# Kernel optimization log

Measured on AMD Instinct MI355X. Metric: run time of the kernel, lower is better.

The kernel has to match this reference:

```python
import jax, jax.numpy as jnp
import numpy as np

B, N, D, H = 8, 1024, 768, 12
HD = D // H


def setup_inputs() -> dict:
    key = jax.random.key(0)
    ks = jax.random.split(key, 13)
    s = 0.02
    return {
        "q": jax.random.normal(ks[0], (B, N, D), jnp.float32),
        "k": jax.random.normal(ks[1], (B, N, D), jnp.float32),
        "v": jax.random.normal(ks[2], (B, N, D), jnp.float32),
        "attn_bias": jax.random.normal(ks[3], (B, H, N, N), jnp.float32),
        "attn_mask": jnp.ones((B, N, N), jnp.int32),
        "Wq": jax.random.normal(ks[4], (D, D), jnp.float32) * s,
        "bq": jnp.zeros((D,), jnp.float32),
        "Wk": jax.random.normal(ks[5], (D, D), jnp.float32) * s,
        "bk": jnp.zeros((D,), jnp.float32),
        "Wv": jax.random.normal(ks[6], (D, D), jnp.float32) * s,
        "bv": jnp.zeros((D,), jnp.float32),
        "Wo": jax.random.normal(ks[7], (D, D), jnp.float32) * s,
        "bo": jnp.zeros((D,), jnp.float32),
    }


def reference(q, k, v, attn_bias, attn_mask, Wq, bq, Wk, bk, Wv, bv, Wo, bo):
    scale = jnp.sqrt(jnp.float32(HD))
    # projections; nn.Linear computes x @ W.T + b
    qh = (q @ Wq.T + bq).reshape(B, N, H, HD).transpose(0, 2, 1, 3)  # [B,H,N,hd]
    kh = (k @ Wk.T + bk).reshape(B, N, H, HD).transpose(0, 2, 1, 3)
    vh = (v @ Wv.T + bv).reshape(B, N, H, HD).transpose(0, 2, 1, 3)
    attn = jnp.einsum("bhqd,bhkd->bhqk", qh, kh) / scale
    attn = attn + attn_bias  # Graphormer edge/spatial bias
    attn = jnp.where(attn_mask[:, None, :, :] == 0, -jnp.inf, attn)
    attn = jax.nn.softmax(attn, axis=-1)
    out = jnp.einsum("bhqk,bhkd->bhqd", attn, vh)  # [B,H,N,hd]
    out = out.transpose(0, 2, 1, 3).reshape(B, N, D)
    return out @ Wo.T + bo
```

## Files before the change

### kernel.cpp

```cpp
#include <hip/hip_runtime.h>
#include <hip/hip_bf16.h>

using f32x4  = __attribute__((ext_vector_type(4))) float;
using i32x4  = __attribute__((ext_vector_type(4))) int;
using bf16x8 = __attribute__((ext_vector_type(8))) short;
using bf16x4 = __attribute__((ext_vector_type(4))) short;

constexpr int BATCH = 8, SEQ = 1024, DIM = 768, NHEAD = 12, HDIM = 64;
constexpr int MROWS = BATCH * SEQ;

__device__ __forceinline__ short f2bf(float f) {
    union { float f; unsigned u; } x; x.f = f;
    unsigned r = (x.u + 0x7fffu + ((x.u >> 16) & 1u)) >> 16;
    return (short)r;
}
__device__ __forceinline__ float fexp2(float x) { return __builtin_amdgcn_exp2f(x); }

template <typename AT, int OMODE>
__global__ __launch_bounds__(256)
void gemm_bt(const AT* __restrict__ A, const float* __restrict__ W,
             const float* __restrict__ bias, void* __restrict__ Cout, float oscale) {
    constexpr int K  = DIM;
    constexpr int NT = DIM / 128;
    __shared__ short As[128][72];
    __shared__ short Bs[128][72];

    const int bm = blockIdx.x / NT, bn = blockIdx.x % NT;
    const int m0 = bm * 128, n0 = bn * 128;
    const int t = threadIdx.x;
    const int lane = t & 63, w = t >> 6;
    const int wm = (w >> 1) * 64, wn = (w & 1) * 64;
    const int l16 = lane & 15, lg = lane >> 4;

    const int sr = t >> 1, sc = (t & 1) * 16;

    f32x4 acc[4][4] = {};

    for (int k0 = 0; k0 < K; k0 += 32) {
        __syncthreads();
        if constexpr (sizeof(AT) == 4) {
            const float* ap = (const float*)A + (long)(m0 + sr) * K + k0 + sc;
            float tmp[16];
            *(f32x4*)&tmp[0]  = *(const f32x4*)(ap + 0);
            *(f32x4*)&tmp[4]  = *(const f32x4*)(ap + 4);
            *(f32x4*)&tmp[8]  = *(const f32x4*)(ap + 8);
            *(f32x4*)&tmp[12] = *(const f32x4*)(ap + 12);
            short tb[16];
            #pragma unroll
            for (int j = 0; j < 16; ++j) tb[j] = f2bf(tmp[j]);
            *(bf16x8*)&As[sr][sc]     = *(bf16x8*)&tb[0];
            *(bf16x8*)&As[sr][sc + 8] = *(bf16x8*)&tb[8];
        } else {
            const short* ap = (const short*)A + (long)(m0 + sr) * K + k0 + sc;
            *(bf16x8*)&As[sr][sc]     = *(const bf16x8*)(ap);
            *(bf16x8*)&As[sr][sc + 8] = *(const bf16x8*)(ap + 8);
        }
        {
            const float* wp = W + (long)(n0 + sr) * K + k0 + sc;
            float tmp[16];
            *(f32x4*)&tmp[0]  = *(const f32x4*)(wp + 0);
            *(f32x4*)&tmp[4]  = *(const f32x4*)(wp + 4);
            *(f32x4*)&tmp[8]  = *(const f32x4*)(wp + 8);
            *(f32x4*)&tmp[12] = *(const f32x4*)(wp + 12);
            short tb[16];
            #pragma unroll
            for (int j = 0; j < 16; ++j) tb[j] = f2bf(tmp[j]);
            *(bf16x8*)&Bs[sr][sc]     = *(bf16x8*)&tb[0];
            *(bf16x8*)&Bs[sr][sc + 8] = *(bf16x8*)&tb[8];
        }
        __syncthreads();

        bf16x8 af[4], bfg[4];
        const int kc = lg * 8;
        #pragma unroll
        for (int mi = 0; mi < 4; ++mi)
            af[mi] = *(const bf16x8*)&As[wm + mi * 16 + l16][kc];
        #pragma unroll
        for (int ni = 0; ni < 4; ++ni)
            bfg[ni] = *(const bf16x8*)&Bs[wn + ni * 16 + l16][kc];
        #pragma unroll
        for (int mi = 0; mi < 4; ++mi)
            #pragma unroll
            for (int ni = 0; ni < 4; ++ni)
                acc[mi][ni] = __builtin_amdgcn_mfma_f32_16x16x32_bf16(
                    af[mi], bfg[ni], acc[mi][ni], 0, 0, 0);
    }

    #pragma unroll
    for (int mi = 0; mi < 4; ++mi) {
        const int row = m0 + wm + mi * 16 + lg * 4;
        #pragma unroll
        for (int ni = 0; ni < 4; ++ni) {
            const int col = n0 + wn + ni * 16 + l16;
            const float bv = bias[col];
            #pragma unroll
            for (int j = 0; j < 4; ++j) {
                float val = (acc[mi][ni][j] + bv) * oscale;
                if constexpr (OMODE == 0) {
                    ((short*)Cout)[(long)(row + j) * DIM + col] = f2bf(val);
                } else if constexpr (OMODE == 1) {
                    ((float*)Cout)[(long)(row + j) * DIM + col] = val;
                } else {
                    const int bb = row / SEQ;
                    const int tok = (row % SEQ) + j;
                    const int hh = col >> 6, dd = col & 63;
                    const long base = ((long)(bb * NHEAD + hh) * 16 + (tok >> 6)) * 4096;
                    if constexpr (OMODE == 2)
                        ((short*)Cout)[base + dd * 64 + (tok & 63)] = f2bf(val);
                    else
                        ((short*)Cout)[base + (tok & 63) * 64 + dd] = f2bf(val);
                }
            }
        }
    }
}

__global__ __launch_bounds__(256)
void attn_kernel(const short* __restrict__ Qp, const short* __restrict__ Kt,
                 const short* __restrict__ Vt, const float* __restrict__ bias,
                 const int* __restrict__ mask, short* __restrict__ Op) {
    __shared__ float Bsm[64][68];
    __shared__ short Ks[64][72];
    __shared__ short Vs[64][72];
    __shared__ short Ps[4][16][72];

    const int d = blockIdx.x;
    const int lgc = (d & 7) * 192 + (d >> 3);
    const int qt = lgc & 15, pair = lgc >> 4;
    const int h = pair % NHEAD, b = pair / NHEAD;

    const int t = threadIdx.x, lane = t & 63, w = t >> 6;
    const int l16 = lane & 15, lg = lane >> 4;
    const int ql = w * 16 + l16;

    const int qrow = qt * 64 + ql;
    const short* qptr = Qp + (long)(b * SEQ + qrow) * DIM + h * HDIM + lg * 8;
    const bf16x8 qf0 = *(const bf16x8*)qptr;
    const bf16x8 qf1 = *(const bf16x8*)(qptr + 32);

    const short* ktile = Kt + (long)pair * 16 * 4096;
    const short* vtile = Vt + (long)pair * 16 * 4096;

    const int srow = t >> 4, scol = (t & 15) * 4;
    const float* bst = bias + ((long)pair * SEQ + qt * 64 + srow) * SEQ + scol;
    const int*   mst = mask + ((long)b * SEQ + qt * 64 + srow) * SEQ + scol;

    const int kr = t >> 3, kc = (t & 7) * 8;

    f32x4 acc_o[4] = {};
    float m_run = -1e30f, l_run = 0.f;
    constexpr float L2E = 1.4426950408889634f;

    f32x4 br[4]; i32x4 mr[4]; bf16x8 kst0, kst1, vst0, vst1;

    {
        #pragma unroll
        for (int i = 0; i < 4; ++i) {
            br[i] = *(const f32x4*)(bst + (long)i * 16 * SEQ);
            mr[i] = *(const i32x4*)(mst + (long)i * 16 * SEQ);
        }
        kst0 = *(const bf16x8*)(ktile + t * 8);
        kst1 = *(const bf16x8*)(ktile + t * 8 + 2048);
        vst0 = *(const bf16x8*)(vtile + t * 8);
        vst1 = *(const bf16x8*)(vtile + t * 8 + 2048);
        #pragma unroll
        for (int i = 0; i < 4; ++i) {
            f32x4 o;
            #pragma unroll
            for (int j = 0; j < 4; ++j) o[j] = mr[i][j] ? br[i][j] : -1e30f;
            *(f32x4*)&Bsm[i * 16 + srow][scol] = o;
        }
        *(bf16x8*)&Ks[kr][kc]      = kst0;
        *(bf16x8*)&Ks[kr + 32][kc] = kst1;
        *(bf16x8*)&Vs[kr][kc]      = vst0;
        *(bf16x8*)&Vs[kr + 32][kc] = vst1;
    }
    __syncthreads();

    for (int kt = 0; kt < 16; ++kt) {
        if (kt < 15) {
            #pragma unroll
            for (int i = 0; i < 4; ++i) {
                br[i] = *(const f32x4*)(bst + (long)i * 16 * SEQ + (kt + 1) * 64);
                mr[i] = *(const i32x4*)(mst + (long)i * 16 * SEQ + (kt + 1) * 64);
            }
            const short* kp = ktile + (kt + 1) * 4096 + t * 8;
            const short* vp = vtile + (kt + 1) * 4096 + t * 8;
            kst0 = *(const bf16x8*)kp;
            kst1 = *(const bf16x8*)(kp + 2048);
            vst0 = *(const bf16x8*)vp;
            vst1 = *(const bf16x8*)(vp + 2048);
        }

        f32x4 s[4];
        #pragma unroll
        for (int c = 0; c < 4; ++c) {
            const bf16x8 kb0 = *(const bf16x8*)&Ks[c * 16 + l16][lg * 8];
            const bf16x8 kb1 = *(const bf16x8*)&Ks[c * 16 + l16][32 + lg * 8];
            f32x4 ci = *(const f32x4*)&Bsm[ql][c * 16 + lg * 4];
            ci   = __builtin_amdgcn_mfma_f32_16x16x32_bf16(kb0, qf0, ci, 0, 0, 0);
            s[c] = __builtin_amdgcn_mfma_f32_16x16x32_bf16(kb1, qf1, ci, 0, 0, 0);
        }

        bf16x8 vb0[4], vb1[4];
        #pragma unroll
        for (int df = 0; df < 4; ++df) {
            vb0[df] = *(const bf16x8*)&Vs[df * 16 + l16][lg * 8];
            vb1[df] = *(const bf16x8*)&Vs[df * 16 + l16][32 + lg * 8];
        }

        float mt = -1e30f;
        #pragma unroll
        for (int c = 0; c < 4; ++c)
            #pragma unroll
            for (int j = 0; j < 4; ++j)
                mt = fmaxf(mt, s[c][j]);
        mt = fmaxf(mt, __shfl_xor(mt, 16));
        mt = fmaxf(mt, __shfl_xor(mt, 32));
        const float mn = fmaxf(m_run, mt);
        const float alpha = fexp2((m_run - mn) * L2E);
        m_run = mn;
        const float nm = -mn * L2E;

        float lt = 0.f;
        #pragma unroll
        for (int c = 0; c < 4; ++c) {
            bf16x4 pk;
            #pragma unroll
            for (int j = 0; j < 4; ++j) {
                const float e = fexp2(fmaf(s[c][j], L2E, nm));
                lt += e;
                pk[j] = f2bf(e);
            }
            *(bf16x4*)&Ps[w][l16][c * 16 + lg * 4] = pk;
        }
        lt += __shfl_xor(lt, 16);
        lt += __shfl_xor(lt, 32);
        l_run = l_run * alpha + lt;

        float al[4];
        #pragma unroll
        for (int j = 0; j < 4; ++j) al[j] = __shfl(alpha, lg * 4 + j);
        #pragma unroll
        for (int df = 0; df < 4; ++df)
            #pragma unroll
            for (int j = 0; j < 4; ++j)
                acc_o[df][j] *= al[j];

        const bf16x8 pa0 = *(const bf16x8*)&Ps[w][l16][lg * 8];
        const bf16x8 pa1 = *(const bf16x8*)&Ps[w][l16][32 + lg * 8];

        #pragma unroll
        for (int df = 0; df < 4; ++df) {
            acc_o[df] = __builtin_amdgcn_mfma_f32_16x16x32_bf16(pa0, vb0[df], acc_o[df], 0, 0, 0);
            acc_o[df] = __builtin_amdgcn_mfma_f32_16x16x32_bf16(pa1, vb1[df], acc_o[df], 0, 0, 0);
        }

        if (kt < 15) {
            __syncthreads();
            #pragma unroll
            for (int i = 0; i < 4; ++i) {
                f32x4 o;
                #pragma unroll
                for (int j = 0; j < 4; ++j) o[j] = mr[i][j] ? br[i][j] : -1e30f;
                *(f32x4*)&Bsm[i * 16 + srow][scol] = o;
            }
            *(bf16x8*)&Ks[kr][kc]      = kst0;
            *(bf16x8*)&Ks[kr + 32][kc] = kst1;
            *(bf16x8*)&Vs[kr][kc]      = vst0;
            *(bf16x8*)&Vs[kr + 32][kc] = vst1;
            __syncthreads();
        }
    }

    float linv[4];
    #pragma unroll
    for (int j = 0; j < 4; ++j)
        linv[j] = 1.f / fmaxf(__shfl(l_run, lg * 4 + j), 1e-20f);

    #pragma unroll
    for (int df = 0; df < 4; ++df) {
        #pragma unroll
        for (int j = 0; j < 4; ++j) {
            const float val = acc_o[df][j] * linv[j];
            const int row = b * SEQ + qt * 64 + w * 16 + lg * 4 + j;
            const int col = h * HDIM + df * 16 + l16;
            Op[(long)row * DIM + col] = f2bf(val);
        }
    }
}

extern "C" void kernel_launch(void* const* d_in, const int* in_sizes, int n_in,
                              void* d_out, int out_size, void* d_ws, size_t ws_size,
                              hipStream_t stream) {
    const float* q         = (const float*)d_in[0];
    const float* k         = (const float*)d_in[1];
    const float* v         = (const float*)d_in[2];
    const float* attn_bias = (const float*)d_in[3];
    const int*   attn_mask = (const int*)d_in[4];
    const float* Wq = (const float*)d_in[5];
    const float* bq = (const float*)d_in[6];
    const float* Wk = (const float*)d_in[7];
    const float* bk = (const float*)d_in[8];
    const float* Wv = (const float*)d_in[9];
    const float* bv = (const float*)d_in[10];
    const float* Wo = (const float*)d_in[11];
    const float* bo = (const float*)d_in[12];
    float* out = (float*)d_out;

    short* Qp = (short*)d_ws;
    short* Kp = Qp + (long)MROWS * DIM;
    short* Vp = Kp + (long)MROWS * DIM;
    short* Op = Vp + (long)MROWS * DIM;

    const dim3 blk(256);
    const int gemm_grid = (MROWS / 128) * (DIM / 128);

    gemm_bt<float, 0><<<gemm_grid, blk, 0, stream>>>(q, Wq, bq, Qp, 0.125f);
    gemm_bt<float, 3><<<gemm_grid, blk, 0, stream>>>(k, Wk, bk, Kp, 1.0f);
    gemm_bt<float, 2><<<gemm_grid, blk, 0, stream>>>(v, Wv, bv, Vp, 1.0f);

    const int attn_grid = BATCH * NHEAD * (SEQ / 64);
    attn_kernel<<<attn_grid, blk, 0, stream>>>(Qp, Kp, Vp, attn_bias, attn_mask, Op);

    gemm_bt<short, 1><<<gemm_grid, blk, 0, stream>>>(Op, Wo, bo, out, 1.0f);
}
```

Baseline: 292.4 us.

## Pre-convert inputs and weights to bf16, register-prefetch GEMM tiles, double-buffer attention loads

Adds separate conversion kernels that turn q/k/v and all four weight matrices into bf16 once per call. The GEMMs then load bf16 directly and prefetch the next K-tile into registers while the current one is computed. The attention kernel gets a two-deep register prefetch of bias and mask, with nontemporal loads for the bias. Launch bounds now request 4 and 3 blocks per CU. The conversion pass adds an extra read-write sweep over the activations, which may cost more than the per-tile conversion it replaces. The attention kernel dominates and streams 400MB of bias, so it likely stays memory bound.

```diff
diff --git a/kernel.cpp b/kernel.cpp
--- a/kernel.cpp
+++ b/kernel.cpp
@@ -16,10 +16,47 @@
 }
 __device__ __forceinline__ float fexp2(float x) { return __builtin_amdgcn_exp2f(x); }
 
-template <typename AT, int OMODE>
+__device__ __forceinline__ bf16x8 cvt8(const float* p) {
+    const f32x4 x0 = *(const f32x4*)p;
+    const f32x4 x1 = *(const f32x4*)(p + 4);
+    bf16x8 r;
+    #pragma unroll
+    for (int j = 0; j < 4; ++j) { r[j] = f2bf(x0[j]); r[4 + j] = f2bf(x1[j]); }
+    return r;
+}
+
 __global__ __launch_bounds__(256)
-void gemm_bt(const AT* __restrict__ A, const float* __restrict__ W,
-             const float* __restrict__ bias, void* __restrict__ Cout, float oscale) {
+void cvt3(const float* __restrict__ a, const float* __restrict__ b,
+          const float* __restrict__ c, short* __restrict__ oa,
+          short* __restrict__ ob, short* __restrict__ oc, int n8) {
+    const int stride = gridDim.x * 256;
+    for (int i = blockIdx.x * 256 + threadIdx.x; i < n8; i += stride) {
+        const long base = (long)i * 8;
+        *(bf16x8*)(oa + base) = cvt8(a + base);
+        *(bf16x8*)(ob + base) = cvt8(b + base);
+        *(bf16x8*)(oc + base) = cvt8(c + base);
+    }
+}
+
+__global__ __launch_bounds__(256)
+void cvt4(const float* __restrict__ a, const float* __restrict__ b,
+          const float* __restrict__ c, const float* __restrict__ d,
+          short* __restrict__ oa, short* __restrict__ ob,
+          short* __restrict__ oc, short* __restrict__ od, int n8) {
+    const int stride = gridDim.x * 256;
+    for (int i = blockIdx.x * 256 + threadIdx.x; i < n8; i += stride) {
+        const long base = (long)i * 8;
+        *(bf16x8*)(oa + base) = cvt8(a + base);
+        *(bf16x8*)(ob + base) = cvt8(b + base);
+        *(bf16x8*)(oc + base) = cvt8(c + base);
+        *(bf16x8*)(od + base) = cvt8(d + base);
+    }
+}
+
+template <int OMODE>
+__global__ __launch_bounds__(256, 4)
+void gemm_bf16(const short* __restrict__ A, const short* __restrict__ W,
+               const float* __restrict__ bias, void* __restrict__ Cout, float oscale) {
     constexpr int K  = DIM;
     constexpr int NT = DIM / 128;
     __shared__ short As[128][72];
@@ -33,40 +70,26 @@
     const int l16 = lane & 15, lg = lane >> 4;
 
     const int sr = t >> 1, sc = (t & 1) * 16;
+    const short* aptr = A + (long)(m0 + sr) * K + sc;
+    const short* wptr = W + (long)(n0 + sr) * K + sc;
+
+    bf16x8 ra0 = *(const bf16x8*)(aptr);
+    bf16x8 ra1 = *(const bf16x8*)(aptr + 8);
+    bf16x8 rw0 = *(const bf16x8*)(wptr);
+    bf16x8 rw1 = *(const bf16x8*)(wptr + 8);
 
     f32x4 acc[4][4] = {};
 
     for (int k0 = 0; k0 < K; k0 += 32) {
-        __syncthreads();
-        if constexpr (sizeof(AT) == 4) {
-            const float* ap = (const float*)A + (long)(m0 + sr) * K + k0 + sc;
-            float tmp[16];
-            *(f32x4*)&tmp[0]  = *(const f32x4*)(ap + 0);
-            *(f32x4*)&tmp[4]  = *(const f32x4*)(ap + 4);
-            *(f32x4*)&tmp[8]  = *(const f32x4*)(ap + 8);
-            *(f32x4*)&tmp[12] = *(const f32x4*)(ap + 12);
-            short tb[16];
-            #pragma unroll
-            for (int j = 0; j < 16; ++j) tb[j] = f2bf(tmp[j]);
-            *(bf16x8*)&As[sr][sc]     = *(bf16x8*)&tb[0];
-            *(bf16x8*)&As[sr][sc + 8] = *(bf16x8*)&tb[8];
-        } else {
-            const short* ap = (const short*)A + (long)(m0 + sr) * K + k0 + sc;
-            *(bf16x8*)&As[sr][sc]     = *(const bf16x8*)(ap);
-            *(bf16x8*)&As[sr][sc + 8] = *(const bf16x8*)(ap + 8);
-        }
-        {
-            const float* wp = W + (long)(n0 + sr) * K + k0 + sc;
-            float tmp[16];
-            *(f32x4*)&tmp[0]  = *(const f32x4*)(wp + 0);
-            *(f32x4*)&tmp[4]  = *(const f32x4*)(wp + 4);
-            *(f32x4*)&tmp[8]  = *(const f32x4*)(wp + 8);
-            *(f32x4*)&tmp[12] = *(const f32x4*)(wp + 12);
-            short tb[16];
-            #pragma unroll
-            for (int j = 0; j < 16; ++j) tb[j] = f2bf(tmp[j]);
-            *(bf16x8*)&Bs[sr][sc]     = *(bf16x8*)&tb[0];
-            *(bf16x8*)&Bs[sr][sc + 8] = *(bf16x8*)&tb[8];
+        *(bf16x8*)&As[sr][sc]     = ra0;
+        *(bf16x8*)&As[sr][sc + 8] = ra1;
+        *(bf16x8*)&Bs[sr][sc]     = rw0;
+        *(bf16x8*)&Bs[sr][sc + 8] = rw1;
+        if (k0 + 32 < K) {
+            ra0 = *(const bf16x8*)(aptr + k0 + 32);
+            ra1 = *(const bf16x8*)(aptr + k0 + 40);
+            rw0 = *(const bf16x8*)(wptr + k0 + 32);
+            rw1 = *(const bf16x8*)(wptr + k0 + 40);
         }
         __syncthreads();
 
@@ -84,6 +107,7 @@
             for (int ni = 0; ni < 4; ++ni)
                 acc[mi][ni] = __builtin_amdgcn_mfma_f32_16x16x32_bf16(
                     af[mi], bfg[ni], acc[mi][ni], 0, 0, 0);
+        __syncthreads();
     }
 
     #pragma unroll
@@ -115,7 +139,7 @@
     }
 }
 
-__global__ __launch_bounds__(256)
+__global__ __launch_bounds__(256, 3)
 void attn_kernel(const short* __restrict__ Qp, const short* __restrict__ Kt,
                  const short* __restrict__ Vt, const float* __restrict__ bias,
                  const int* __restrict__ mask, short* __restrict__ Op) {
@@ -151,18 +175,26 @@
     float m_run = -1e30f, l_run = 0.f;
     constexpr float L2E = 1.4426950408889634f;
 
-    f32x4 br[4]; i32x4 mr[4]; bf16x8 kst0, kst1, vst0, vst1;
-
-    {
+    f32x4 brA[4], brB[4];
+    i32x4 mrA[4], mrB[4];
+    bf16x8 kst0, kst1, vst0, vst1;
+
+    auto issue_bm = [&](int kt, f32x4 (&br)[4], i32x4 (&mr)[4]) {
         #pragma unroll
         for (int i = 0; i < 4; ++i) {
-            br[i] = *(const f32x4*)(bst + (long)i * 16 * SEQ);
-            mr[i] = *(const i32x4*)(mst + (long)i * 16 * SEQ);
-        }
-        kst0 = *(const bf16x8*)(ktile + t * 8);
-        kst1 = *(const bf16x8*)(ktile + t * 8 + 2048);
-        vst0 = *(const bf16x8*)(vtile + t * 8);
-        vst1 = *(const bf16x8*)(vtile + t * 8 + 2048);
+            br[i] = __builtin_nontemporal_load((const f32x4*)(bst + (long)i * 16 * SEQ + kt * 64));
+            mr[i] = *(const i32x4*)(mst + (long)i * 16 * SEQ + kt * 64);
+        }
+    };
+    auto issue_kv = [&](int kt) {
+        const short* kp = ktile + kt * 4096 + t * 8;
+        const short* vp = vtile + kt * 4096 + t * 8;
+        kst0 = *(const bf16x8*)kp;
+        kst1 = *(const bf16x8*)(kp + 2048);
+        vst0 = *(const bf16x8*)vp;
+        vst1 = *(const bf16x8*)(vp + 2048);
+    };
+    auto write_bm = [&](f32x4 (&br)[4], i32x4 (&mr)[4]) {
         #pragma unroll
         for (int i = 0; i < 4; ++i) {
             f32x4 o;
@@ -170,28 +202,15 @@
             for (int j = 0; j < 4; ++j) o[j] = mr[i][j] ? br[i][j] : -1e30f;
             *(f32x4*)&Bsm[i * 16 + srow][scol] = o;
         }
+    };
+    auto write_kv = [&]() {
         *(bf16x8*)&Ks[kr][kc]      = kst0;
         *(bf16x8*)&Ks[kr + 32][kc] = kst1;
         *(bf16x8*)&Vs[kr][kc]      = vst0;
         *(bf16x8*)&Vs[kr + 32][kc] = vst1;
-    }
-    __syncthreads();
-
-    for (int kt = 0; kt < 16; ++kt) {
-        if (kt < 15) {
-            #pragma unroll
-            for (int i = 0; i < 4; ++i) {
-                br[i] = *(const f32x4*)(bst + (long)i * 16 * SEQ + (kt + 1) * 64);
-                mr[i] = *(const i32x4*)(mst + (long)i * 16 * SEQ + (kt + 1) * 64);
-            }
-            const short* kp = ktile + (kt + 1) * 4096 + t * 8;
-            const short* vp = vtile + (kt + 1) * 4096 + t * 8;
-            kst0 = *(const bf16x8*)kp;
-            kst1 = *(const bf16x8*)(kp + 2048);
-            vst0 = *(const bf16x8*)vp;
-            vst1 = *(const bf16x8*)(vp + 2048);
-        }
-
+    };
+
+    auto compute = [&]() {
         f32x4 s[4];
         #pragma unroll
         for (int c = 0; c < 4; ++c) {
@@ -201,7 +220,6 @@
             ci   = __builtin_amdgcn_mfma_f32_16x16x32_bf16(kb0, qf0, ci, 0, 0, 0);
             s[c] = __builtin_amdgcn_mfma_f32_16x16x32_bf16(kb1, qf1, ci, 0, 0, 0);
         }
-
         bf16x8 vb0[4], vb1[4];
         #pragma unroll
         for (int df = 0; df < 4; ++df) {
@@ -249,26 +267,37 @@
 
         const bf16x8 pa0 = *(const bf16x8*)&Ps[w][l16][lg * 8];
         const bf16x8 pa1 = *(const bf16x8*)&Ps[w][l16][32 + lg * 8];
-
         #pragma unroll
         for (int df = 0; df < 4; ++df) {
             acc_o[df] = __builtin_amdgcn_mfma_f32_16x16x32_bf16(pa0, vb0[df], acc_o[df], 0, 0, 0);
             acc_o[df] = __builtin_amdgcn_mfma_f32_16x16x32_bf16(pa1, vb1[df], acc_o[df], 0, 0, 0);
         }
-
-        if (kt < 15) {
+    };
+
+    issue_bm(0, brA, mrA);
+    issue_kv(0);
+    write_bm(brA, mrA);
+    write_kv();
+    issue_bm(1, brA, mrA);
+    __syncthreads();
+
+    for (int kk = 0; kk < 16; kk += 2) {
+        if (kk + 2 < 16) issue_bm(kk + 2, brB, mrB);
+        if (kk + 1 < 16) issue_kv(kk + 1);
+        compute();
+        if (kk + 1 < 16) {
             __syncthreads();
-            #pragma unroll
-            for (int i = 0; i < 4; ++i) {
-                f32x4 o;
-                #pragma unroll
-                for (int j = 0; j < 4; ++j) o[j] = mr[i][j] ? br[i][j] : -1e30f;
-                *(f32x4*)&Bsm[i * 16 + srow][scol] = o;
-            }
-            *(bf16x8*)&Ks[kr][kc]      = kst0;
-            *(bf16x8*)&Ks[kr + 32][kc] = kst1;
-            *(bf16x8*)&Vs[kr][kc]      = vst0;
-            *(bf16x8*)&Vs[kr + 32][kc] = vst1;
+            write_bm(brA, mrA);
+            write_kv();
+            __syncthreads();
+        }
+        if (kk + 3 < 16) issue_bm(kk + 3, brA, mrA);
+        if (kk + 2 < 16) issue_kv(kk + 2);
+        compute();
+        if (kk + 2 < 16) {
+            __syncthreads();
+            write_bm(brB, mrB);
+            write_kv();
             __syncthreads();
         }
     }
@@ -308,20 +337,32 @@
     const float* bo = (const float*)d_in[12];
     float* out = (float*)d_out;
 
-    short* Qp = (short*)d_ws;
-    short* Kp = Qp + (long)MROWS * DIM;
-    short* Vp = Kp + (long)MROWS * DIM;
-    short* Op = Vp + (long)MROWS * DIM;
+    const long NED = (long)MROWS * DIM;
+    const long WED = (long)DIM * DIM;
+    short* Qp  = (short*)d_ws;
+    short* Kp  = Qp + NED;
+    short* Vp  = Kp + NED;
+    short* Op  = Vp + NED;
+    short* qb  = Op + NED;
+    short* kb  = qb + NED;
+    short* vb  = kb + NED;
+    short* Wqb = vb + NED;
+    short* Wkb = Wqb + WED;
+    short* Wvb = Wkb + WED;
+    short* Wob = Wvb + WED;
 
     const dim3 blk(256);
+
+    cvt3<<<2048, blk, 0, stream>>>(q, k, v, qb, kb, vb, (int)(NED / 8));
+    cvt4<<<288, blk, 0, stream>>>(Wq, Wk, Wv, Wo, Wqb, Wkb, Wvb, Wob, (int)(WED / 8));
+
     const int gemm_grid = (MROWS / 128) * (DIM / 128);
-
-    gemm_bt<float, 0><<<gemm_grid, blk, 0, stream>>>(q, Wq, bq, Qp, 0.125f);
-    gemm_bt<float, 3><<<gemm_grid, blk, 0, stream>>>(k, Wk, bk, Kp, 1.0f);
-    gemm_bt<float, 2><<<gemm_grid, blk, 0, stream>>>(v, Wv, bv, Vp, 1.0f);
+    gemm_bf16<0><<<gemm_grid, blk, 0, stream>>>(qb, Wqb, bq, Qp, 0.125f);
+    gemm_bf16<3><<<gemm_grid, blk, 0, stream>>>(kb, Wkb, bk, Kp, 1.0f);
+    gemm_bf16<2><<<gemm_grid, blk, 0, stream>>>(vb, Wvb, bv, Vp, 1.0f);
 
     const int attn_grid = BATCH * NHEAD * (SEQ / 64);
     attn_kernel<<<attn_grid, blk, 0, stream>>>(Qp, Kp, Vp, attn_bias, attn_mask, Op);
 
-    gemm_bt<short, 1><<<gemm_grid, blk, 0, stream>>>(Op, Wo, bo, out, 1.0f);
-}
+    gemm_bf16<1><<<gemm_grid, blk, 0, stream>>>(Op, Wob, bo, out, 1.0f);
+}
```

After: 379.0 us. 1.3x slower.
